# Optimization experiments

Hardware: AMD Instinct MI355X
Metric: run time of the kernel (lower is better)

Reference implementation:

```python
import jax, jax.numpy as jnp
import numpy as np

S, B, C = 7, 2, 3
LAMBDA_NOOBJ = 0.5
LAMBDA_COORD = 5.0
EPS = 1e-6


def _iou(box_a, box_b):
    # boxes in center format [x, y, w, h]; shapes [..., 4]
    ax1 = box_a[..., 0] - box_a[..., 2] / 2
    ay1 = box_a[..., 1] - box_a[..., 3] / 2
    ax2 = box_a[..., 0] + box_a[..., 2] / 2
    ay2 = box_a[..., 1] + box_a[..., 3] / 2
    bx1 = box_b[..., 0] - box_b[..., 2] / 2
    by1 = box_b[..., 1] - box_b[..., 3] / 2
    bx2 = box_b[..., 0] + box_b[..., 2] / 2
    by2 = box_b[..., 1] + box_b[..., 3] / 2
    iw = jnp.clip(jnp.minimum(ax2, bx2) - jnp.maximum(ax1, bx1), 0.0)
    ih = jnp.clip(jnp.minimum(ay2, by2) - jnp.maximum(ay1, by1), 0.0)
    inter = iw * ih
    union = (ax2 - ax1) * (ay2 - ay1) + (bx2 - bx1) * (by2 - by1) - inter
    return inter / (union + EPS)


def setup_inputs() -> dict:
    key = jax.random.key(0)
    k1, k2, k3, k4 = jax.random.split(key, 4)
    batch = 32768
    predictions = jax.random.normal(k1, (batch, S, S, 5 * B + C), dtype=jnp.float32)
    obj = (jax.random.uniform(k2, (batch, S, S, 1)) < 0.1).astype(jnp.float32)
    boxes = jax.random.uniform(k3, (batch, S, S, 4), minval=0.05, maxval=0.95)
    cls = jax.random.uniform(k4, (batch, S, S, C))
    target = jnp.concatenate([obj, boxes, cls], axis=-1)
    return {"predictions": predictions, "target": target}


def reference(predictions, target):
    batch = target.shape[0]
    obj = target[..., 0] == 1.0          # [b,S,S] bool
    t_box = target[..., 1:5]
    t_cls = target[..., 5:]

    box1 = predictions[..., 0:5]
    box2 = predictions[..., 5:10]
    p_cls = predictions[..., 10:]

    iou1 = _iou(predictions[..., 1:5], t_box)
    iou2 = _iou(predictions[..., 6:10], t_box)
    pick1 = iou1 > iou2                   # torch branch: iou1 > iou2 -> box1 else box2
    iou = jnp.where(pick1, iou1, iou2)
    sel = jnp.where(pick1[..., None], box1, box2)    # [b,S,S,5]
    unsel = jnp.where(pick1[..., None], box2, box1)

    m = obj.astype(predictions.dtype)     # [b,S,S]

    loss_xy = jnp.sum(m[..., None] * (sel[..., 1:3] - t_box[..., 0:2]) ** 2)
    sel_wh = sel[..., 3:5]
    wh_term = jnp.sign(sel_wh) * jnp.sqrt(jnp.abs(sel_wh)) - jnp.sqrt(t_box[..., 2:4])
    loss_wh = jnp.sum(m[..., None] * wh_term ** 2)
    loss_obj = jnp.sum(m * (sel[..., 0] - iou) ** 2)
    loss_class = jnp.sum(m[..., None] * (p_cls - t_cls) ** 2)

    noobj_both = predictions[..., 0] ** 2 + predictions[..., 5] ** 2
    loss_no_obj = jnp.sum(m * unsel[..., 0] ** 2) + jnp.sum((1.0 - m) * noobj_both)

    loss = LAMBDA_COORD * (loss_xy + loss_wh) + loss_obj + LAMBDA_NOOBJ * loss_no_obj + loss_class
    return loss / batch
```

## Files before the change

kernel.cpp:

```cpp
#include <hip/hip_runtime.h>


static constexpr int PRED_C = 13;
static constexpr int TGT_C  = 8;
static constexpr float L_NOOBJ = 0.5f;
static constexpr float L_COORD = 5.0f;
static constexpr float EPSI = 1e-6f;

__device__ __forceinline__ float iou_f(float ax, float ay, float aw, float ah,
                                       float bx, float by, float bw, float bh) {
    float ax1 = ax - aw * 0.5f, ax2 = ax + aw * 0.5f;
    float ay1 = ay - ah * 0.5f, ay2 = ay + ah * 0.5f;
    float bx1 = bx - bw * 0.5f, bx2 = bx + bw * 0.5f;
    float by1 = by - bh * 0.5f, by2 = by + bh * 0.5f;
    float iw = fmaxf(fminf(ax2, bx2) - fmaxf(ax1, bx1), 0.0f);
    float ih = fmaxf(fminf(ay2, by2) - fmaxf(ay1, by1), 0.0f);
    float inter = iw * ih;
    float uni = (ax2 - ax1) * (ay2 - ay1) + (bx2 - bx1) * (by2 - by1) - inter;
    return inter / (uni + EPSI);
}

__device__ __forceinline__ float cell_loss(const float* __restrict__ p,
                                           const float* __restrict__ tg) {
    float m  = (tg[0] == 1.0f) ? 1.0f : 0.0f;
    float tx = tg[1], ty = tg[2], tw = tg[3], th = tg[4];

    float b1c = p[0],  b1x = p[1],  b1y = p[2],  b1w = p[3], b1h = p[4];
    float b2c = p[5],  b2x = p[6],  b2y = p[7],  b2w = p[8], b2h = p[9];

    float i1 = iou_f(b1x, b1y, b1w, b1h, tx, ty, tw, th);
    float i2 = iou_f(b2x, b2y, b2w, b2h, tx, ty, tw, th);
    bool pick1 = i1 > i2;
    float iou = pick1 ? i1 : i2;
    float sc  = pick1 ? b1c : b2c;
    float sx  = pick1 ? b1x : b2x;
    float sy  = pick1 ? b1y : b2y;
    float sw  = pick1 ? b1w : b2w;
    float sh  = pick1 ? b1h : b2h;
    float uc  = pick1 ? b2c : b1c;

    float dx = sx - tx, dy = sy - ty;
    float dw = copysignf(sqrtf(fabsf(sw)), sw) - sqrtf(tw);
    float dh = copysignf(sqrtf(fabsf(sh)), sh) - sqrtf(th);
    float l_coord = dx * dx + dy * dy + dw * dw + dh * dh;

    float doj = sc - iou;
    float d0 = p[10] - tg[5], d1 = p[11] - tg[6], d2 = p[12] - tg[7];
    float l_cls = d0 * d0 + d1 * d1 + d2 * d2;
    float l_noobj = m * uc * uc + (1.0f - m) * (b1c * b1c + b2c * b2c);

    return m * (L_COORD * l_coord + doj * doj + l_cls) + L_NOOBJ * l_noobj;
}

__global__ __launch_bounds__(256) void yolo_main(const float* __restrict__ pred,
                                                 const float* __restrict__ tgt,
                                                 float* __restrict__ partial,
                                                 long long ncells) {
    __shared__ float wsum[4];
    const int t = threadIdx.x;
    const long long tid = (long long)blockIdx.x * 256 + t;
    const long long c0 = tid * 4;

    float acc = 0.0f;
    if (c0 + 4 <= ncells) {
        const float4* p4 = (const float4*)pred + tid * 13;
        float4 P[13];
#pragma unroll
        for (int i = 0; i < 13; ++i) P[i] = p4[i];
        const float4* t4 = (const float4*)tgt + tid * 8;
        float4 T[8];
#pragma unroll
        for (int i = 0; i < 8; ++i) T[i] = t4[i];

        const float* pf = (const float*)P;
        const float* tf = (const float*)T;
#pragma unroll
        for (int c = 0; c < 4; ++c)
            acc += cell_loss(pf + c * PRED_C, tf + c * TGT_C);
    } else {
        for (int c = 0; c < 4; ++c) {
            long long cell = c0 + c;
            if (cell < ncells) {
                float pb[PRED_C], tb[TGT_C];
                for (int i = 0; i < PRED_C; ++i) pb[i] = pred[cell * PRED_C + i];
                for (int i = 0; i < TGT_C; ++i)  tb[i] = tgt[cell * TGT_C + i];
                acc += cell_loss(pb, tb);
            }
        }
    }

#pragma unroll
    for (int off = 32; off > 0; off >>= 1)
        acc += __shfl_down(acc, off, 64);
    if ((t & 63) == 0) wsum[t >> 6] = acc;
    __syncthreads();
    if (t == 0) partial[blockIdx.x] = (wsum[0] + wsum[1]) + (wsum[2] + wsum[3]);
}

__global__ __launch_bounds__(256) void yolo_reduce(const float* __restrict__ partial,
                                                   float* __restrict__ out,
                                                   int nblocks, float inv_batch) {
    __shared__ float wsum[4];
    int t = threadIdx.x;
    float v = 0.0f;
    for (int i = t; i < nblocks; i += 256) v += partial[i];
#pragma unroll
    for (int off = 32; off > 0; off >>= 1)
        v += __shfl_down(v, off, 64);
    if ((t & 63) == 0) wsum[t >> 6] = v;
    __syncthreads();
    if (t == 0) out[0] = ((wsum[0] + wsum[1]) + (wsum[2] + wsum[3])) * inv_batch;
}

extern "C" void kernel_launch(void* const* d_in, const int* in_sizes, int n_in,
                              void* d_out, int out_size, void* d_ws, size_t ws_size,
                              hipStream_t stream) {
    const float* pred = (const float*)d_in[0];
    const float* tgt  = (const float*)d_in[1];
    float* out = (float*)d_out;
    float* partial = (float*)d_ws;

    long long ncells = (long long)in_sizes[1] / TGT_C;
    long long batch  = ncells / 49;
    float inv_batch  = 1.0f / (float)batch;

    long long nthreads = (ncells + 3) / 4;
    int nblocks = (int)((nthreads + 255) / 256);

    yolo_main<<<nblocks, 256, 0, stream>>>(pred, tgt, partial, ncells);
    yolo_reduce<<<1, 256, 0, stream>>>(partial, out, nblocks, inv_batch);
}
```

Baseline: 175.0 us.

## Stage predictions through LDS via direct global-to-LDS loads in grid-stride tiles

Each wave now handles 64-cell tiles in a grid-stride loop over a fixed 2048-block grid. The 13-float prediction records are copied coalesced straight into shared memory with global_load_lds, and each lane then reads its own cell from LDS. This replaces per-thread 13×float4 register loads, which used many registers and gave strided access. The cost is a manual waitcnt, LDS bank conflicts from the stride-13 reads, and a reliance on the tile staying aligned to the wave's buffer layout.

```diff
diff --git a/kernel.cpp b/kernel.cpp
--- a/kernel.cpp
+++ b/kernel.cpp
@@ -6,6 +6,13 @@
 static constexpr float L_NOOBJ = 0.5f;
 static constexpr float L_COORD = 5.0f;
 static constexpr float EPSI = 1e-6f;
+
+static constexpr int NBLOCKS = 2048;
+static constexpr int WTILE   = 64;
+static constexpr int WTILE_F = WTILE * PRED_C;
+
+typedef const __attribute__((address_space(1))) unsigned int* gp1_t;
+typedef __attribute__((address_space(3))) unsigned int*       lp3_t;
 
 __device__ __forceinline__ float iou_f(float ax, float ay, float aw, float ah,
                                        float bx, float by, float bw, float bh) {
@@ -55,31 +62,51 @@
 __global__ __launch_bounds__(256) void yolo_main(const float* __restrict__ pred,
                                                  const float* __restrict__ tgt,
                                                  float* __restrict__ partial,
-                                                 long long ncells) {
+                                                 long long ntiles, long long ncells) {
+    __shared__ float sp[4][WTILE_F];
     __shared__ float wsum[4];
-    const int t = threadIdx.x;
-    const long long tid = (long long)blockIdx.x * 256 + t;
-    const long long c0 = tid * 4;
+
+    const int t    = threadIdx.x;
+    const int lane = t & 63;
+    const int wave = t >> 6;
+    const long long gw0    = (long long)blockIdx.x * 4 + wave;
+    const long long nwaves = (long long)gridDim.x * 4;
 
     float acc = 0.0f;
-    if (c0 + 4 <= ncells) {
-        const float4* p4 = (const float4*)pred + tid * 13;
-        float4 P[13];
+
+    for (long long tile = gw0; tile < ntiles; tile += nwaves) {
+        const long long cbase = tile * WTILE;
+
+        if (cbase + WTILE <= ncells) {
+            const float* gp = pred + cbase * (long long)PRED_C;
 #pragma unroll
-        for (int i = 0; i < 13; ++i) P[i] = p4[i];
-        const float4* t4 = (const float4*)tgt + tid * 8;
-        float4 T[8];
+            for (int r = 0; r < 3; ++r) {
+                __builtin_amdgcn_global_load_lds(
+                    (gp1_t)(gp + (size_t)(r * 64 + lane) * 4),
+                    (lp3_t)(&sp[wave][r * 256]),
+                    16, 0, 0);
+            }
+            if (lane < 16) {
+                __builtin_amdgcn_global_load_lds(
+                    (gp1_t)(gp + (size_t)(192 + lane) * 4),
+                    (lp3_t)(&sp[wave][768]),
+                    16, 0, 0);
+            }
+            const float4* t4 = (const float4*)(tgt + (cbase + lane) * (long long)TGT_C);
+            float4 T0 = t4[0];
+            float4 T1 = t4[1];
+
+            __builtin_amdgcn_s_waitcnt(0x0F70);
+
+            float tg[TGT_C] = {T0.x, T0.y, T0.z, T0.w, T1.x, T1.y, T1.z, T1.w};
+            float pb[PRED_C];
 #pragma unroll
-        for (int i = 0; i < 8; ++i) T[i] = t4[i];
+            for (int i = 0; i < PRED_C; ++i)
+                pb[i] = sp[wave][lane * PRED_C + i];
 
-        const float* pf = (const float*)P;
-        const float* tf = (const float*)T;
-#pragma unroll
-        for (int c = 0; c < 4; ++c)
-            acc += cell_loss(pf + c * PRED_C, tf + c * TGT_C);
-    } else {
-        for (int c = 0; c < 4; ++c) {
-            long long cell = c0 + c;
+            acc += cell_loss(pb, tg);
+        } else {
+            long long cell = cbase + lane;
             if (cell < ncells) {
                 float pb[PRED_C], tb[TGT_C];
                 for (int i = 0; i < PRED_C; ++i) pb[i] = pred[cell * PRED_C + i];
@@ -92,7 +119,7 @@
 #pragma unroll
     for (int off = 32; off > 0; off >>= 1)
         acc += __shfl_down(acc, off, 64);
-    if ((t & 63) == 0) wsum[t >> 6] = acc;
+    if (lane == 0) wsum[wave] = acc;
     __syncthreads();
     if (t == 0) partial[blockIdx.x] = (wsum[0] + wsum[1]) + (wsum[2] + wsum[3]);
 }
@@ -123,10 +150,8 @@
     long long ncells = (long long)in_sizes[1] / TGT_C;
     long long batch  = ncells / 49;
     float inv_batch  = 1.0f / (float)batch;
+    long long ntiles = (ncells + WTILE - 1) / WTILE;
 
-    long long nthreads = (ncells + 3) / 4;
-    int nblocks = (int)((nthreads + 255) / 256);
-
-    yolo_main<<<nblocks, 256, 0, stream>>>(pred, tgt, partial, ncells);
-    yolo_reduce<<<1, 256, 0, stream>>>(partial, out, nblocks, inv_batch);
+    yolo_main<<<NBLOCKS, 256, 0, stream>>>(pred, tgt, partial, ntiles, ncells);
+    yolo_reduce<<<1, 256, 0, stream>>>(partial, out, NBLOCKS, inv_batch);
 }
```

Result: faster. 161.5 us (-7.7%).

## Coalesce prediction loads via LDS staging in persistent, prefetching waves

Applied to the files above, without the earlier changes.

Replaces the per-thread strided float4 loads (13 contiguous float4 per thread) with wave-cooperative coalesced loads of a 256-cell tile into LDS. Each thread then reads its cells' predictions back from shared memory. The grid becomes a fixed 768-block persistent loop in which each wave software-prefetches the next tile into registers while computing the current one. This aims to improve global memory coalescing and overlap loads with compute, at the cost of LDS traffic, possible bank conflicts from the stride-13 reads, and higher register pressure.

```diff
diff --git a/kernel.cpp b/kernel.cpp
--- a/kernel.cpp
+++ b/kernel.cpp
@@ -6,6 +6,10 @@
 static constexpr float L_NOOBJ = 0.5f;
 static constexpr float L_COORD = 5.0f;
 static constexpr float EPSI = 1e-6f;
+
+static constexpr int TILE    = 256;
+static constexpr int SLAB4   = TILE * PRED_C / 4;
+static constexpr int NBLOCKS = 768;
 
 __device__ __forceinline__ float iou_f(float ax, float ay, float aw, float ah,
                                        float bx, float by, float bw, float bh) {
@@ -21,9 +25,9 @@
 }
 
 __device__ __forceinline__ float cell_loss(const float* __restrict__ p,
-                                           const float* __restrict__ tg) {
-    float m  = (tg[0] == 1.0f) ? 1.0f : 0.0f;
-    float tx = tg[1], ty = tg[2], tw = tg[3], th = tg[4];
+                                           float4 ta, float4 tb) {
+    float m  = (ta.x == 1.0f) ? 1.0f : 0.0f;
+    float tx = ta.y, ty = ta.z, tw = ta.w, th = tb.x;
 
     float b1c = p[0],  b1x = p[1],  b1y = p[2],  b1w = p[3], b1h = p[4];
     float b2c = p[5],  b2x = p[6],  b2y = p[7],  b2w = p[8], b2h = p[9];
@@ -45,7 +49,7 @@
     float l_coord = dx * dx + dy * dy + dw * dw + dh * dh;
 
     float doj = sc - iou;
-    float d0 = p[10] - tg[5], d1 = p[11] - tg[6], d2 = p[12] - tg[7];
+    float d0 = p[10] - tb.y, d1 = p[11] - tb.z, d2 = p[12] - tb.w;
     float l_cls = d0 * d0 + d1 * d1 + d2 * d2;
     float l_noobj = m * uc * uc + (1.0f - m) * (b1c * b1c + b2c * b2c);
 
@@ -55,44 +59,89 @@
 __global__ __launch_bounds__(256) void yolo_main(const float* __restrict__ pred,
                                                  const float* __restrict__ tgt,
                                                  float* __restrict__ partial,
-                                                 long long ncells) {
+                                                 long long ntiles, long long ncells) {
+    __shared__ float4 sp4[4][SLAB4];
     __shared__ float wsum[4];
-    const int t = threadIdx.x;
-    const long long tid = (long long)blockIdx.x * 256 + t;
-    const long long c0 = tid * 4;
+
+    const int t    = threadIdx.x;
+    const int lane = t & 63;
+    const int wave = t >> 6;
+    float4* slab4 = sp4[wave];
+    const float* slabf = (const float*)slab4;
+
+    const long long nw = (long long)gridDim.x * 4;
+    long long tile = (long long)blockIdx.x * 4 + wave;
 
     float acc = 0.0f;
-    if (c0 + 4 <= ncells) {
-        const float4* p4 = (const float4*)pred + tid * 13;
-        float4 P[13];
+    float4 P[13];
+    float4 T[8];
+
+    auto issue = [&](long long tl) {
+        const long long cb = tl * TILE;
+        const float4* gp4 = (const float4*)(pred + cb * PRED_C);
 #pragma unroll
-        for (int i = 0; i < 13; ++i) P[i] = p4[i];
-        const float4* t4 = (const float4*)tgt + tid * 8;
-        float4 T[8];
+        for (int r = 0; r < 13; ++r) P[r] = gp4[r * 64 + lane];
 #pragma unroll
-        for (int i = 0; i < 8; ++i) T[i] = t4[i];
+        for (int k = 0; k < 4; ++k) {
+            const float4* gt4 = (const float4*)(tgt + (cb + 64 * k + lane) * TGT_C);
+            T[2 * k]     = gt4[0];
+            T[2 * k + 1] = gt4[1];
+        }
+    };
+    auto full = [&](long long tl) { return (tl + 1) * TILE <= ncells; };
 
-        const float* pf = (const float*)P;
-        const float* tf = (const float*)T;
+    bool curFull = false;
+    if (tile < ntiles) {
+        curFull = full(tile);
+        if (curFull) issue(tile);
+    }
+
+    while (tile < ntiles) {
+        const long long next = tile + nw;
+        const bool nextFull = (next < ntiles) && full(next);
+
+        if (curFull) {
 #pragma unroll
-        for (int c = 0; c < 4; ++c)
-            acc += cell_loss(pf + c * PRED_C, tf + c * TGT_C);
-    } else {
-        for (int c = 0; c < 4; ++c) {
-            long long cell = c0 + c;
-            if (cell < ncells) {
-                float pb[PRED_C], tb[TGT_C];
-                for (int i = 0; i < PRED_C; ++i) pb[i] = pred[cell * PRED_C + i];
-                for (int i = 0; i < TGT_C; ++i)  tb[i] = tgt[cell * TGT_C + i];
-                acc += cell_loss(pb, tb);
+            for (int r = 0; r < 13; ++r) slab4[r * 64 + lane] = P[r];
+            float4 ta0 = T[0], tb0 = T[1], ta1 = T[2], tb1 = T[3];
+            float4 ta2 = T[4], tb2 = T[5], ta3 = T[6], tb3 = T[7];
+
+            if (nextFull) issue(next);
+
+            float pb[PRED_C];
+#pragma unroll
+            for (int i = 0; i < PRED_C; ++i) pb[i] = slabf[lane * PRED_C + i];
+            acc += cell_loss(pb, ta0, tb0);
+#pragma unroll
+            for (int i = 0; i < PRED_C; ++i) pb[i] = slabf[(64 + lane) * PRED_C + i];
+            acc += cell_loss(pb, ta1, tb1);
+#pragma unroll
+            for (int i = 0; i < PRED_C; ++i) pb[i] = slabf[(128 + lane) * PRED_C + i];
+            acc += cell_loss(pb, ta2, tb2);
+#pragma unroll
+            for (int i = 0; i < PRED_C; ++i) pb[i] = slabf[(192 + lane) * PRED_C + i];
+            acc += cell_loss(pb, ta3, tb3);
+        } else {
+            const long long cb = tile * TILE;
+            for (int k = 0; k < 4; ++k) {
+                long long cell = cb + 64 * k + lane;
+                if (cell < ncells) {
+                    float pb[PRED_C];
+                    for (int i = 0; i < PRED_C; ++i) pb[i] = pred[cell * PRED_C + i];
+                    const float4* gt4 = (const float4*)(tgt + cell * TGT_C);
+                    acc += cell_loss(pb, gt4[0], gt4[1]);
+                }
             }
+            if (nextFull) issue(next);
         }
+        curFull = nextFull;
+        tile = next;
     }
 
 #pragma unroll
     for (int off = 32; off > 0; off >>= 1)
         acc += __shfl_down(acc, off, 64);
-    if ((t & 63) == 0) wsum[t >> 6] = acc;
+    if (lane == 0) wsum[wave] = acc;
     __syncthreads();
     if (t == 0) partial[blockIdx.x] = (wsum[0] + wsum[1]) + (wsum[2] + wsum[3]);
 }
@@ -123,10 +172,8 @@
     long long ncells = (long long)in_sizes[1] / TGT_C;
     long long batch  = ncells / 49;
     float inv_batch  = 1.0f / (float)batch;
+    long long ntiles = (ncells + TILE - 1) / TILE;
 
-    long long nthreads = (ncells + 3) / 4;
-    int nblocks = (int)((nthreads + 255) / 256);
-
-    yolo_main<<<nblocks, 256, 0, stream>>>(pred, tgt, partial, ncells);
-    yolo_reduce<<<1, 256, 0, stream>>>(partial, out, nblocks, inv_batch);
+    yolo_main<<<NBLOCKS, 256, 0, stream>>>(pred, tgt, partial, ntiles, ncells);
+    yolo_reduce<<<1, 256, 0, stream>>>(partial, out, NBLOCKS, inv_batch);
 }
```

Measured after the change: 193.7 us. 1.11x slower.

## Stage prediction loads through per-wave LDS slabs for coalesced global reads

Applied to the files above, without the earlier changes.

Each wavefront now loads a contiguous 256-cell slab of predictions with lane-strided float4 reads, writes it to shared memory, and reads back each lane's cell. This replaces the old scheme where every thread read 13 consecutive float4s, which gave strided, poorly coalesced global accesses. Targets are read as two float4 per cell, and the work split becomes 64-cell strides per lane with launch bounds asking for 3 blocks per CU. The cost is 53KB of LDS per block, which limits occupancy, plus the LDS round-trip with 13-float strided reads that may cause bank conflicts.

```diff
diff --git a/kernel.cpp b/kernel.cpp
--- a/kernel.cpp
+++ b/kernel.cpp
@@ -6,6 +6,9 @@
 static constexpr float L_NOOBJ = 0.5f;
 static constexpr float L_COORD = 5.0f;
 static constexpr float EPSI = 1e-6f;
+
+static constexpr int WCELLS = 256;
+static constexpr int SLAB4  = WCELLS * PRED_C / 4;
 
 __device__ __forceinline__ float iou_f(float ax, float ay, float aw, float ah,
                                        float bx, float by, float bw, float bh) {
@@ -21,9 +24,9 @@
 }
 
 __device__ __forceinline__ float cell_loss(const float* __restrict__ p,
-                                           const float* __restrict__ tg) {
-    float m  = (tg[0] == 1.0f) ? 1.0f : 0.0f;
-    float tx = tg[1], ty = tg[2], tw = tg[3], th = tg[4];
+                                           float4 ta, float4 tb) {
+    float m  = (ta.x == 1.0f) ? 1.0f : 0.0f;
+    float tx = ta.y, ty = ta.z, tw = ta.w, th = tb.x;
 
     float b1c = p[0],  b1x = p[1],  b1y = p[2],  b1w = p[3], b1h = p[4];
     float b2c = p[5],  b2x = p[6],  b2y = p[7],  b2w = p[8], b2h = p[9];
@@ -45,46 +48,86 @@
     float l_coord = dx * dx + dy * dy + dw * dw + dh * dh;
 
     float doj = sc - iou;
-    float d0 = p[10] - tg[5], d1 = p[11] - tg[6], d2 = p[12] - tg[7];
+    float d0 = p[10] - tb.y, d1 = p[11] - tb.z, d2 = p[12] - tb.w;
     float l_cls = d0 * d0 + d1 * d1 + d2 * d2;
     float l_noobj = m * uc * uc + (1.0f - m) * (b1c * b1c + b2c * b2c);
 
     return m * (L_COORD * l_coord + doj * doj + l_cls) + L_NOOBJ * l_noobj;
 }
 
-__global__ __launch_bounds__(256) void yolo_main(const float* __restrict__ pred,
-                                                 const float* __restrict__ tgt,
-                                                 float* __restrict__ partial,
-                                                 long long ncells) {
+__global__ __launch_bounds__(256, 3) void yolo_main(const float* __restrict__ pred,
+                                                    const float* __restrict__ tgt,
+                                                    float* __restrict__ partial,
+                                                    long long ncells) {
+    __shared__ float4 sp4[4][SLAB4];
     __shared__ float wsum[4];
-    const int t = threadIdx.x;
-    const long long tid = (long long)blockIdx.x * 256 + t;
-    const long long c0 = tid * 4;
+
+    const int t    = threadIdx.x;
+    const int lane = t & 63;
+    const int wave = t >> 6;
+    float4* slab4 = sp4[wave];
+    const float* slabf = (const float*)slab4;
+
+    const long long gw    = (long long)blockIdx.x * 4 + wave;
+    const long long cbase = gw * WCELLS;
 
     float acc = 0.0f;
-    if (c0 + 4 <= ncells) {
-        const float4* p4 = (const float4*)pred + tid * 13;
-        float4 P[13];
-#pragma unroll
-        for (int i = 0; i < 13; ++i) P[i] = p4[i];
-        const float4* t4 = (const float4*)tgt + tid * 8;
+
+    if (cbase + WCELLS <= ncells) {
+        const float4* gp4 = (const float4*)pred + gw * SLAB4;
+        float4 P0  = gp4[0 * 64 + lane];
+        float4 P1  = gp4[1 * 64 + lane];
+        float4 P2  = gp4[2 * 64 + lane];
+        float4 P3  = gp4[3 * 64 + lane];
+        float4 P4  = gp4[4 * 64 + lane];
+        float4 P5  = gp4[5 * 64 + lane];
+        float4 P6  = gp4[6 * 64 + lane];
+        float4 P7  = gp4[7 * 64 + lane];
+        float4 P8  = gp4[8 * 64 + lane];
+        float4 P9  = gp4[9 * 64 + lane];
+        float4 P10 = gp4[10 * 64 + lane];
+        float4 P11 = gp4[11 * 64 + lane];
+        float4 P12 = gp4[12 * 64 + lane];
+
+        const float4* gt4 = (const float4*)tgt;
         float4 T[8];
 #pragma unroll
-        for (int i = 0; i < 8; ++i) T[i] = t4[i];
+        for (int k = 0; k < 4; ++k) {
+            long long cell = cbase + 64 * k + lane;
+            T[2 * k]     = gt4[cell * 2];
+            T[2 * k + 1] = gt4[cell * 2 + 1];
+        }
 
-        const float* pf = (const float*)P;
-        const float* tf = (const float*)T;
+        slab4[0 * 64 + lane]  = P0;
+        slab4[1 * 64 + lane]  = P1;
+        slab4[2 * 64 + lane]  = P2;
+        slab4[3 * 64 + lane]  = P3;
+        slab4[4 * 64 + lane]  = P4;
+        slab4[5 * 64 + lane]  = P5;
+        slab4[6 * 64 + lane]  = P6;
+        slab4[7 * 64 + lane]  = P7;
+        slab4[8 * 64 + lane]  = P8;
+        slab4[9 * 64 + lane]  = P9;
+        slab4[10 * 64 + lane] = P10;
+        slab4[11 * 64 + lane] = P11;
+        slab4[12 * 64 + lane] = P12;
+
+        float pb[PRED_C];
 #pragma unroll
-        for (int c = 0; c < 4; ++c)
-            acc += cell_loss(pf + c * PRED_C, tf + c * TGT_C);
+        for (int k = 0; k < 4; ++k) {
+#pragma unroll
+            for (int i = 0; i < PRED_C; ++i)
+                pb[i] = slabf[(64 * k + lane) * PRED_C + i];
+            acc += cell_loss(pb, T[2 * k], T[2 * k + 1]);
+        }
     } else {
-        for (int c = 0; c < 4; ++c) {
-            long long cell = c0 + c;
+        for (int k = 0; k < 4; ++k) {
+            long long cell = cbase + 64 * k + lane;
             if (cell < ncells) {
-                float pb[PRED_C], tb[TGT_C];
+                float pb[PRED_C];
                 for (int i = 0; i < PRED_C; ++i) pb[i] = pred[cell * PRED_C + i];
-                for (int i = 0; i < TGT_C; ++i)  tb[i] = tgt[cell * TGT_C + i];
-                acc += cell_loss(pb, tb);
+                const float4* gt4 = (const float4*)(tgt + cell * TGT_C);
+                acc += cell_loss(pb, gt4[0], gt4[1]);
             }
         }
     }
@@ -92,7 +135,7 @@
 #pragma unroll
     for (int off = 32; off > 0; off >>= 1)
         acc += __shfl_down(acc, off, 64);
-    if ((t & 63) == 0) wsum[t >> 6] = acc;
+    if (lane == 0) wsum[wave] = acc;
     __syncthreads();
     if (t == 0) partial[blockIdx.x] = (wsum[0] + wsum[1]) + (wsum[2] + wsum[3]);
 }
@@ -124,8 +167,8 @@
     long long batch  = ncells / 49;
     float inv_batch  = 1.0f / (float)batch;
 
-    long long nthreads = (ncells + 3) / 4;
-    int nblocks = (int)((nthreads + 255) / 256);
+    long long cells_per_block = 4LL * WCELLS;
+    int nblocks = (int)((ncells + cells_per_block - 1) / cells_per_block);
 
     yolo_main<<<nblocks, 256, 0, stream>>>(pred, tgt, partial, ncells);
     yolo_reduce<<<1, 256, 0, stream>>>(partial, out, nblocks, inv_batch);
```

After: 161.5 us. 1.08x faster.
